# Kernel tuning notes

Hardware: AMD Instinct MI355X
Metric: run time of the kernel (lower is better)

## Reference

```python
import jax, jax.numpy as jnp
import numpy as np

V, E, H = 32000, 256, 256  # vocab, embed dim, encoder hidden (decoder hidden = 2H)
B, S, T = 64, 32, 32


def gru_cell(x, h, W_ih, W_hh, b_ih, b_hh):
    # PyTorch GRU cell math. x: (B, in), h: (B, Hd)
    gi = x @ W_ih.T + b_ih
    gh = h @ W_hh.T + b_hh
    i_r, i_z, i_n = jnp.split(gi, 3, axis=-1)
    h_r, h_z, h_n = jnp.split(gh, 3, axis=-1)
    r = jax.nn.sigmoid(i_r + h_r)
    z = jax.nn.sigmoid(i_z + h_z)
    n = jnp.tanh(i_n + r * h_n)
    return (1.0 - z) * n + z * h


def setup_inputs() -> dict:
    key = jax.random.key(0)
    ks = jax.random.split(key, 20)
    s = 0.05
    emb_enc = jax.random.normal(ks[0], (V, E), jnp.float32) * s
    emb_enc = emb_enc.at[0].set(0.0)  # padding_idx=0
    emb_dec = jax.random.normal(ks[1], (V, E), jnp.float32) * s
    emb_dec = emb_dec.at[0].set(0.0)
    inp = {
        "src": jax.random.randint(ks[2], (B, S), 0, V),
        "trg": jax.random.randint(ks[3], (B, T), 0, V),
        "emb_enc": emb_enc,
        # encoder bidirectional GRU (single layer)
        "W_ih_f": jax.random.normal(ks[4], (3 * H, E), jnp.float32) * s,
        "W_hh_f": jax.random.normal(ks[5], (3 * H, H), jnp.float32) * s,
        "b_ih_f": jnp.zeros((3 * H,), jnp.float32),
        "b_hh_f": jnp.zeros((3 * H,), jnp.float32),
        "W_ih_b": jax.random.normal(ks[6], (3 * H, E), jnp.float32) * s,
        "W_hh_b": jax.random.normal(ks[7], (3 * H, H), jnp.float32) * s,
        "b_ih_b": jnp.zeros((3 * H,), jnp.float32),
        "b_hh_b": jnp.zeros((3 * H,), jnp.float32),
        "emb_dec": emb_dec,
        # decoder GRU: input E + 2H, hidden 2H
        "W_ih_d": jax.random.normal(ks[8], (3 * 2 * H, E + 2 * H), jnp.float32) * s,
        "W_hh_d": jax.random.normal(ks[9], (3 * 2 * H, 2 * H), jnp.float32) * s,
        "b_ih_d": jnp.zeros((3 * 2 * H,), jnp.float32),
        "b_hh_d": jnp.zeros((3 * 2 * H,), jnp.float32),
        "fc_W": jax.random.normal(ks[10], (V, 2 * H), jnp.float32) * s,
        "fc_b": jnp.zeros((V,), jnp.float32),
    }
    return inp


def _forward(src, trg, emb_enc, W_ih_f, W_hh_f, b_ih_f, b_hh_f,
             W_ih_b, W_hh_b, b_ih_b, b_hh_b, emb_dec,
             W_ih_d, W_hh_d, b_ih_d, b_hh_d, fc_W, fc_b):
    b, s = src.shape
    t = trg.shape[1]
    x = emb_enc[src]                      # (B,S,E)
    xs = jnp.swapaxes(x, 0, 1)            # (S,B,E)
    h0 = jnp.zeros((b, H), x.dtype)

    def fstep(h, xt):
        h = gru_cell(xt, h, W_ih_f, W_hh_f, b_ih_f, b_hh_f)
        return h, None

    def bstep(h, xt):
        h = gru_cell(xt, h, W_ih_b, W_hh_b, b_ih_b, b_hh_b)
        return h, None

    hf, _ = jax.lax.scan(fstep, h0, xs)
    hb, _ = jax.lax.scan(bstep, h0, xs[::-1])
    context = jnp.concatenate([hf, hb], axis=-1)   # (B,2H) = final bidir hidden

    # teacher_forcing_ratio = 1.0 -> decoder input at step t is trg[:, t-1]
    dec_in = jnp.swapaxes(trg[:, :-1], 0, 1)       # (T-1, B)

    def dstep(h, tok):
        xt = jnp.concatenate([emb_dec[tok], context], axis=-1)  # (B, E+2H)
        h = gru_cell(xt, h, W_ih_d, W_hh_d, b_ih_d, b_hh_d)
        logits = h @ fc_W.T + fc_b                              # (B, V)
        return h, logits

    _, logits = jax.lax.scan(dstep, context, dec_in)  # (T-1, B, V)
    logits = jnp.swapaxes(logits, 0, 1)                # (B, T-1, V)
    outputs = jnp.concatenate(
        [jnp.zeros((b, 1, fc_W.shape[0]), logits.dtype), logits], axis=1)
    return outputs


def reference(src, trg, emb_enc, W_ih_f, W_hh_f, b_ih_f, b_hh_f,
              W_ih_b, W_hh_b, b_ih_b, b_hh_b, emb_dec,
              W_ih_d, W_hh_d, b_ih_d, b_hh_d, fc_W, fc_b):
    return _forward(src, trg, emb_enc, W_ih_f, W_hh_f, b_ih_f, b_hh_f,
                    W_ih_b, W_hh_b, b_ih_b, b_hh_b, emb_dec,
                    W_ih_d, W_hh_d, b_ih_d, b_hh_d, fc_W, fc_b)
```

## Files before the change

kernel.cpp:

```cpp
#include <hip/hip_runtime.h>
#include <cmath>

typedef _Float16 f16;
typedef _Float16 f16x4 __attribute__((ext_vector_type(4)));
typedef _Float16 f16x8 __attribute__((ext_vector_type(8)));
typedef float f32x4 __attribute__((ext_vector_type(4)));
typedef unsigned u32x4 __attribute__((ext_vector_type(4)));
typedef unsigned long long u64;

static constexpr u64 SENT = 0xFFFFFFFFFFFFFFFFULL;

union V4 { u32x4 u; f16x8 h; };

static constexpr size_t OFF_WIHF = 0;
static constexpr size_t OFF_WHHF = OFF_WIHF + 768UL*256*2;
static constexpr size_t OFF_WIHB = OFF_WHHF + 768UL*256*2;
static constexpr size_t OFF_WHHB = OFF_WIHB + 768UL*256*2;
static constexpr size_t OFF_WIHD = OFF_WHHB + 768UL*256*2;
static constexpr size_t OFF_WHHD = OFF_WIHD + 1536UL*768*2;
static constexpr size_t OFF_FCW  = OFF_WHHD + 1536UL*512*2;
static constexpr size_t OFF_XENC = OFF_FCW  + 32000UL*512*2;
static constexpr size_t OFF_XDEC = OFF_XENC + 2048UL*256*2;
static constexpr size_t OFF_GIF  = OFF_XDEC + 1984UL*256*2;
static constexpr size_t OFF_GIB  = OFF_GIF  + 2048UL*768*4;
static constexpr size_t OFF_GITOK= OFF_GIB  + 2048UL*768*4;
static constexpr size_t OFF_CTX32= OFF_GITOK+ 1984UL*1536*4;
static constexpr size_t OFF_CTX16= OFF_CTX32+ 64UL*512*4;
static constexpr size_t OFF_HPP  = OFF_CTX16+ 64UL*512*2;
static constexpr size_t OFF_HALL = OFF_HPP  + 2UL*32*64*256*2;

__device__ __forceinline__ float sigmoidf_(float x) {
  return __builtin_amdgcn_rcpf(1.f + __expf(-x));
}
__device__ __forceinline__ float tanhf_(float x) {
  float xc = fminf(fmaxf(x, -10.f), 10.f);
  float e = __expf(2.f * xc);
  return (e - 1.f) * __builtin_amdgcn_rcpf(e + 1.f);
}

__device__ __forceinline__ void wait_vm0() {
  asm volatile("s_waitcnt vmcnt(0)" ::: "memory");
  __builtin_amdgcn_sched_barrier(0);
}
__device__ __forceinline__ void sth4(f16* p, float a, float b, float c, float d) {
  union { u64 u; f16 h[4]; } t;
  t.h[0] = (f16)a; t.h[1] = (f16)b; t.h[2] = (f16)c; t.h[3] = (f16)d;
  __hip_atomic_store((u64*)p, t.u, __ATOMIC_RELAXED, __HIP_MEMORY_SCOPE_AGENT);
}

__global__ void k_init(const int* __restrict__ srct, const int* __restrict__ trgt,
                       const float* __restrict__ embe, const float* __restrict__ embd,
                       const float* __restrict__ wihf, const float* __restrict__ whhf,
                       const float* __restrict__ wihb, const float* __restrict__ whhb,
                       const float* __restrict__ wihd, const float* __restrict__ whhd,
                       const float* __restrict__ fcw,
                       f16* dWihf, f16* dWhhf, f16* dWihb, f16* dWhhb,
                       f16* dWihd, f16* dWhhd, f16* dFcw,
                       f16* __restrict__ Xenc, f16* __restrict__ Xdec,
                       f16* __restrict__ hpp, f16* __restrict__ Hall,
                       float* __restrict__ out) {
  int b = blockIdx.x, tid = threadIdx.x;
  if (b < 1024) {
    long t = (long)b * 256 + tid;
    const long stride = 1024L * 256;
    for (long i = t; i < 4032L * 64; i += stride) {
      int row = (int)(i >> 6), j4 = (int)(i & 63);
      const float* e; f16* d; int tok;
      if (row < 2048) {
        int s = row >> 6, bb = row & 63;
        tok = srct[bb * 32 + s]; e = embe; d = Xenc + (long)row * 256;
      } else {
        int rd = row - 2048; int tt = rd >> 6, bb = rd & 63;
        tok = trgt[bb * 32 + tt]; e = embd; d = Xdec + (long)rd * 256;
      }
      float4 v = ((const float4*)(e + (long)tok * 256))[j4];
      f16x4 o; o.x = (f16)v.x; o.y = (f16)v.y; o.z = (f16)v.z; o.w = (f16)v.w;
      ((f16x4*)d)[j4] = o;
    }
    for (long i = t; i < 64L * 8000; i += stride) {
      long bb = i / 8000, j = i % 8000;
      ((float4*)(out + bb * 1024000L))[j] = make_float4(0.f, 0.f, 0.f, 0.f);
    }
    u64* H8 = (u64*)Hall;
    if (t < 253952) H8[t] = SENT;
    u64* P8 = (u64*)hpp;
    if (t < 4096) { P8[t] = 0ULL; P8[131072 + t] = 0ULL; }
    if (t < 126976) { P8[4096 + t] = SENT; P8[131072 + 4096 + t] = SENT; }
  } else {
    long cb = b - 1024;
    const long stride = 4672L * 256;
    for (long i = cb * 256 + tid; i < 4784128L; i += stride) {
      const float* s; f16* d; long j = i;
      if (j < 49152L)        { s = wihf; d = dWihf; }
      else if (j < 98304L)   { s = whhf; d = dWhhf; j -= 49152L; }
      else if (j < 147456L)  { s = wihb; d = dWihb; j -= 98304L; }
      else if (j < 196608L)  { s = whhb; d = dWhhb; j -= 147456L; }
      else if (j < 491520L)  { s = wihd; d = dWihd; j -= 196608L; }
      else if (j < 688128L)  { s = whhd; d = dWhhd; j -= 491520L; }
      else                   { s = fcw;  d = dFcw;  j -= 688128L; }
      float4 v = ((const float4*)s)[j];
      f16x4 o; o.x = (f16)v.x; o.y = (f16)v.y; o.z = (f16)v.z; o.w = (f16)v.w;
      ((f16x4*)d)[j] = o;
    }
  }
}

__device__ __forceinline__ void gemm_body(int bx, int by,
                                          const f16* __restrict__ A, int lda,
                                          const f16* __restrict__ B, int ldb,
                                          const float* __restrict__ bias,
                                          float* __restrict__ C, int ldc, int Ksteps) {
  int m0 = bx * 64, n0 = by * 64;
  int lane = threadIdx.x & 63, w = threadIdx.x >> 6;
  int ar = m0 + w * 16 + (lane & 15);
  int koff = (lane >> 4) * 8;
  f32x4 acc[4] = {};
  for (int ks = 0; ks < Ksteps; ks++) {
    f16x8 a = *(const f16x8*)(A + (size_t)ar * lda + ks * 32 + koff);
#pragma unroll
    for (int ni = 0; ni < 4; ni++) {
      const f16* bp = B + (size_t)(n0 + ni * 16 + (lane & 15)) * ldb + ks * 32 + koff;
      f16x8 bfr = *(const f16x8*)bp;
      acc[ni] = __builtin_amdgcn_mfma_f32_16x16x32_f16(a, bfr, acc[ni], 0, 0, 0);
    }
  }
  int dm = m0 + w * 16 + ((lane >> 4) << 2);
  int dn0 = n0 + (lane & 15);
#pragma unroll
  for (int ni = 0; ni < 4; ni++) {
    int n = dn0 + ni * 16;
    float bv = bias ? bias[n] : 0.f;
#pragma unroll
    for (int r = 0; r < 4; r++) C[(size_t)(dm + r) * ldc + n] = acc[ni][r] + bv;
  }
}

__global__ __launch_bounds__(256) void k_gi(const f16* __restrict__ Xenc, const f16* __restrict__ Xdec,
                                            const f16* __restrict__ Wf, const f16* __restrict__ Wb,
                                            const f16* __restrict__ Wd,
                                            const float* __restrict__ bf, const float* __restrict__ bb,
                                            float* __restrict__ giF, float* __restrict__ giB,
                                            float* __restrict__ giTok) {
  int b = blockIdx.x;
  if (b < 384)      gemm_body(b & 31, b >> 5, Xenc, 256, Wf, 256, bf, giF, 768, 8);
  else if (b < 768) { b -= 384; gemm_body(b & 31, b >> 5, Xenc, 256, Wb, 256, bb, giB, 768, 8); }
  else              { b -= 768; gemm_body(b % 31, b / 31, Xdec, 256, Wd, 768, nullptr, giTok, 1536, 8); }
}

__global__ __launch_bounds__(256, 1) void k_enc(
    const float* __restrict__ giF, const float* __restrict__ giB,
    const f16* __restrict__ WhhF, const f16* __restrict__ WhhB,
    const float* __restrict__ bhhF, const float* __restrict__ bhhB,
    f16* __restrict__ hpp, float* __restrict__ ctx32, f16* __restrict__ ctx16) {
  __shared__ f16 W[96 * 256];
  int wg = blockIdx.x;
  int dir = wg >> 3, ns = wg & 7;
  int tid = threadIdx.x, lane = tid & 63, wv = tid >> 6;
  int mTile = wv;
  const float* gi = dir ? giB : giF;
  const f16* Whh = dir ? WhhB : WhhF;
  const float* bhh = dir ? bhhB : bhhF;
  f16* hb = hpp + (size_t)dir * (32 * 64 * 256);
  int lo = lane & 15, hi = lane >> 4;
  int m = mTile * 16 + lo;
  int jb0 = ns * 32 + hi * 4;

#pragma unroll
  for (int c = 0; c < 12; c++) {
    int seg = c * 256 + tid;
    int row = seg >> 5, ck = seg & 31;
    int q = row >> 5, ii = row & 31;
    f16x8 v = *(const f16x8*)(Whh + (size_t)(q * 256 + ns * 32 + ii) * 256 + ck * 8);
    int col = (ck * 8) ^ ((row & 7) << 3);
    *(f16x8*)&W[row * 256 + col] = v;
  }
  __syncthreads();

  float4 bh[3][2];
#pragma unroll
  for (int q = 0; q < 3; q++)
#pragma unroll
    for (int i = 0; i < 2; i++)
      bh[q][i] = *(const float4*)(bhh + q * 256 + jb0 + i * 16);

  float4 ho[2] = {};
  float4 gcur[3][2];
  {
    int s0 = dir ? 31 : 0;
    const float* g0 = gi + (size_t)s0 * (64 * 768);
#pragma unroll
    for (int q = 0; q < 3; q++)
#pragma unroll
      for (int i = 0; i < 2; i++)
        gcur[q][i] = *(const float4*)(g0 + (size_t)m * 768 + q * 256 + jb0 + i * 16);
  }

  for (int s = 0; s < 32; s++) {
    V4 hv[8];
    const char* hb8 = (const char*)hb + ((size_t)s * 16384 + (size_t)m * 256 + hi * 8) * 2;
    for (;;) {
#pragma unroll
      for (int ks = 0; ks < 8; ks++)
        asm volatile("global_load_dwordx4 %0, %1, off offset:%2 sc0 sc1"
                     : "=&v"(hv[ks].u) : "v"(hb8), "i"(ks * 64));
      wait_vm0();
      unsigned bad = 0;
#pragma unroll
      for (int ks = 0; ks < 8; ks++) {
        bad |= ((hv[ks].u.x & hv[ks].u.y) == 0xFFFFFFFFu);
        bad |= ((hv[ks].u.z & hv[ks].u.w) == 0xFFFFFFFFu);
      }
      if (!__any((int)bad)) break;
      __builtin_amdgcn_s_sleep(1);
    }
    f32x4 acc[3][2] = {};
#pragma unroll
    for (int ks = 0; ks < 8; ks++) {
#pragma unroll
      for (int q = 0; q < 3; q++)
#pragma unroll
        for (int i = 0; i < 2; i++) {
          int row = q * 32 + i * 16 + lo;
          int col = (ks * 32 + hi * 8) ^ ((row & 7) << 3);
          f16x8 w = *(const f16x8*)&W[row * 256 + col];
          acc[q][i] = __builtin_amdgcn_mfma_f32_16x16x32_f16(w, hv[ks].h, acc[q][i], 0, 0, 0);
        }
    }
#pragma unroll
    for (int i = 0; i < 2; i++) {
      float hvv[4];
#pragma unroll
      for (int r2 = 0; r2 < 4; r2++) {
        float rg = sigmoidf_(((const float*)&gcur[0][i])[r2] + acc[0][i][r2] + ((const float*)&bh[0][i])[r2]);
        float zg = sigmoidf_(((const float*)&gcur[1][i])[r2] + acc[1][i][r2] + ((const float*)&bh[1][i])[r2]);
        float ng = tanhf_(((const float*)&gcur[2][i])[r2] + rg * (acc[2][i][r2] + ((const float*)&bh[2][i])[r2]));
        float hprev = ((const float*)&ho[i])[r2];
        hvv[r2] = (1.f - zg) * ng + zg * hprev;
        ((float*)&ho[i])[r2] = hvv[r2];
      }
      if (s < 31) sth4(hb + (size_t)(s + 1) * 16384 + m * 256 + jb0 + i * 16,
                       hvv[0], hvv[1], hvv[2], hvv[3]);
    }
    if (s < 31) {
      int sn = s + 1;
      int sgin = dir ? (31 - sn) : sn;
      const float* gs = gi + (size_t)sgin * (64 * 768);
#pragma unroll
      for (int q = 0; q < 3; q++)
#pragma unroll
        for (int i = 0; i < 2; i++)
          gcur[q][i] = *(const float4*)(gs + (size_t)m * 768 + q * 256 + jb0 + i * 16);
    }
  }
#pragma unroll
  for (int i = 0; i < 2; i++) {
    int c = dir * 256 + jb0 + i * 16;
    *(float4*)(ctx32 + m * 512 + c) = ho[i];
    union { u64 u; f16 h[4]; } t;
#pragma unroll
    for (int r2 = 0; r2 < 4; r2++) t.h[r2] = (f16)((const float*)&ho[i])[r2];
    *(u64*)(ctx16 + m * 512 + c) = t.u;
  }
}

__global__ __launch_bounds__(256, 1) void k_dec(
    const float* __restrict__ giTok, const f16* __restrict__ Wihd, const float* __restrict__ bihd,
    const f16* __restrict__ Whh, const float* __restrict__ bhh,
    const float* __restrict__ ctx32, const f16* __restrict__ ctx16,
    f16* __restrict__ Hall) {
  __shared__ f16 W[48 * 512];
  int cg = blockIdx.x;
  int tid = threadIdx.x, lane = tid & 63, wv = tid >> 6;
  int mTile = wv;
  int lo = lane & 15, hi = lane >> 4;
  int koff = hi * 8;
  int m = mTile * 16 + lo;
  int j0 = cg * 16 + hi * 4;

#pragma unroll
  for (int c = 0; c < 12; c++) {
    int seg = c * 256 + tid;
    int row = seg >> 6, ck = seg & 63;
    int q = row >> 4, ii = row & 15;
    f16x8 v = *(const f16x8*)(Whh + (size_t)(q * 512 + cg * 16 + ii) * 512 + ck * 8);
    int col = (ck * 8) ^ ((row & 7) << 3);
    *(f16x8*)&W[row * 512 + col] = v;
  }

  f32x4 acx[3] = {};
#pragma unroll
  for (int ks = 0; ks < 16; ks++) {
    f16x8 a = *(const f16x8*)(ctx16 + (size_t)m * 512 + ks * 32 + koff);
#pragma unroll
    for (int q = 0; q < 3; q++) {
      f16x8 w = *(const f16x8*)(Wihd + (size_t)(q * 512 + cg * 16 + lo) * 768 + 256 + ks * 32 + koff);
      acx[q] = __builtin_amdgcn_mfma_f32_16x16x32_f16(w, a, acx[q], 0, 0, 0);
    }
  }
  float b0[4], b1[4], bo2[4], bhn[4];
#pragma unroll
  for (int r2 = 0; r2 < 4; r2++) {
    b0[r2]  = acx[0][r2] + bihd[j0 + r2]        + bhh[j0 + r2];
    b1[r2]  = acx[1][r2] + bihd[512 + j0 + r2]  + bhh[512 + j0 + r2];
    bo2[r2] = acx[2][r2] + bihd[1024 + j0 + r2];
    bhn[r2] = bhh[1024 + j0 + r2];
  }
  float4 ho = *(const float4*)(ctx32 + m * 512 + j0);
  float4 gcur[3];
#pragma unroll
  for (int q = 0; q < 3; q++)
    gcur[q] = *(const float4*)(giTok + (size_t)m * 1536 + q * 512 + j0);
  __syncthreads();

  for (int t = 0; t < 31; t++) {
    V4 hv[16];
    if (t == 0) {
      const char* cb = (const char*)ctx16 + ((size_t)m * 512 + hi * 8) * 2;
#pragma unroll
      for (int ks = 0; ks < 16; ks++)
        hv[ks].u = *(const u32x4*)(cb + ks * 64);
    } else {
      const char* hb8 = (const char*)Hall + ((size_t)(t - 1) * 32768 + (size_t)m * 512 + hi * 8) * 2;
      for (;;) {
#pragma unroll
        for (int ks = 0; ks < 16; ks++)
          asm volatile("global_load_dwordx4 %0, %1, off offset:%2 sc0 sc1"
                       : "=&v"(hv[ks].u) : "v"(hb8), "i"(ks * 64));
        wait_vm0();
        unsigned bad = 0;
#pragma unroll
        for (int ks = 0; ks < 16; ks++) {
          bad |= ((hv[ks].u.x & hv[ks].u.y) == 0xFFFFFFFFu);
          bad |= ((hv[ks].u.z & hv[ks].u.w) == 0xFFFFFFFFu);
        }
        if (!__any((int)bad)) break;
        __builtin_amdgcn_s_sleep(1);
      }
    }
    f32x4 acc[3] = {};
#pragma unroll
    for (int ks = 0; ks < 16; ks++) {
#pragma unroll
      for (int q = 0; q < 3; q++) {
        int row = q * 16 + lo;
        int col = (ks * 32 + hi * 8) ^ ((row & 7) << 3);
        f16x8 w = *(const f16x8*)&W[row * 512 + col];
        acc[q] = __builtin_amdgcn_mfma_f32_16x16x32_f16(w, hv[ks].h, acc[q], 0, 0, 0);
      }
    }
    float hvv[4];
#pragma unroll
    for (int r2 = 0; r2 < 4; r2++) {
      float rg = sigmoidf_(((const float*)&gcur[0])[r2] + acc[0][r2] + b0[r2]);
      float zg = sigmoidf_(((const float*)&gcur[1])[r2] + acc[1][r2] + b1[r2]);
      float ng = tanhf_(((const float*)&gcur[2])[r2] + bo2[r2] + rg * (acc[2][r2] + bhn[r2]));
      float hprev = ((const float*)&ho)[r2];
      hvv[r2] = (1.f - zg) * ng + zg * hprev;
      ((float*)&ho)[r2] = hvv[r2];
    }
    sth4(Hall + (size_t)t * 32768 + (size_t)m * 512 + j0, hvv[0], hvv[1], hvv[2], hvv[3]);
    {
      int tn = (t + 1 < 31) ? t + 1 : 30;
      const float* gs = giTok + (size_t)tn * (64 * 1536);
#pragma unroll
      for (int q = 0; q < 3; q++)
        gcur[q] = *(const float4*)(gs + (size_t)m * 1536 + q * 512 + j0);
    }
  }
}

__global__ __launch_bounds__(256, 2) void k_fc(const f16* __restrict__ Hall, const f16* __restrict__ Wfc,
                                               const float* __restrict__ fcb, float* __restrict__ out) {
  __shared__ f16 As[128 * 64];
  __shared__ f16 Bs[128 * 64];
  int bid = blockIdx.x;
  int bx = bid >> 4;
  int by = bid & 15;
  int m0 = by * 128, n0 = bx * 128;
  int tid = threadIdx.x, lane = tid & 63, wv = tid >> 6;
  int wm = wv >> 1, wn = wv & 1;
  f32x4 acc[4][4] = {};
  for (int kk = 0; kk < 8; kk++) {
    f16x8 ra[4], rb[4];
#pragma unroll
    for (int c = 0; c < 4; c++) {
      int seg = c * 256 + tid;
      int row = seg >> 3, ko = (seg & 7) * 8;
      ra[c] = *(const f16x8*)(Hall + (size_t)(m0 + row) * 512 + kk * 64 + ko);
      rb[c] = *(const f16x8*)(Wfc + (size_t)(n0 + row) * 512 + kk * 64 + ko);
    }
    __syncthreads();
#pragma unroll
    for (int c = 0; c < 4; c++) {
      int seg = c * 256 + tid;
      int row = seg >> 3;
      int col = ((seg & 7) * 8) ^ ((row & 7) << 3);
      *(f16x8*)&As[row * 64 + col] = ra[c];
      *(f16x8*)&Bs[row * 64 + col] = rb[c];
    }
    __syncthreads();
#pragma unroll
    for (int ks = 0; ks < 2; ks++) {
      f16x8 af[4], bf[4];
#pragma unroll
      for (int mi = 0; mi < 4; mi++) {
        int row = wm * 64 + mi * 16 + (lane & 15);
        int col = (ks * 32 + (lane >> 4) * 8) ^ ((row & 7) << 3);
        af[mi] = *(const f16x8*)&As[row * 64 + col];
      }
#pragma unroll
      for (int ni = 0; ni < 4; ni++) {
        int row = wn * 64 + ni * 16 + (lane & 15);
        int col = (ks * 32 + (lane >> 4) * 8) ^ ((row & 7) << 3);
        bf[ni] = *(const f16x8*)&Bs[row * 64 + col];
      }
#pragma unroll
      for (int mi = 0; mi < 4; mi++) {
#pragma unroll
        for (int ni = 0; ni < 4; ni++)
          acc[mi][ni] = __builtin_amdgcn_mfma_f32_16x16x32_f16(af[mi], bf[ni], acc[mi][ni], 0, 0, 0);
      }
    }
  }
  int dn0 = n0 + wn * 64 + (lane & 15);
  float bv[4];
#pragma unroll
  for (int ni = 0; ni < 4; ni++) bv[ni] = fcb[dn0 + ni * 16];
#pragma unroll
  for (int mi = 0; mi < 4; mi++) {
    int mbase = m0 + wm * 64 + mi * 16 + ((lane >> 4) << 2);
#pragma unroll
    for (int rr = 0; rr < 4; rr++) {
      int mm = mbase + rr;
      if (mm < 1984) {
        int t = mm >> 6, bb = mm & 63;
        float* orow = out + (size_t)bb * 1024000 + (size_t)(t + 1) * 32000;
#pragma unroll
        for (int ni = 0; ni < 4; ni++)
          __builtin_nontemporal_store(acc[mi][ni][rr] + bv[ni], orow + dn0 + ni * 16);
      }
    }
  }
}

extern "C" void kernel_launch(void* const* d_in, const int* in_sizes, int n_in,
                              void* d_out, int out_size, void* d_ws, size_t ws_size,
                              hipStream_t stream) {
  const int*   srct = (const int*)d_in[0];
  const int*   trgt = (const int*)d_in[1];
  const float* embe = (const float*)d_in[2];
  const float* wihf = (const float*)d_in[3];
  const float* whhf = (const float*)d_in[4];
  const float* bihf = (const float*)d_in[5];
  const float* bhhf = (const float*)d_in[6];
  const float* wihb = (const float*)d_in[7];
  const float* whhb = (const float*)d_in[8];
  const float* bihb = (const float*)d_in[9];
  const float* bhhb = (const float*)d_in[10];
  const float* embd = (const float*)d_in[11];
  const float* wihd = (const float*)d_in[12];
  const float* whhd = (const float*)d_in[13];
  const float* bihd = (const float*)d_in[14];
  const float* bhhd = (const float*)d_in[15];
  const float* fcw  = (const float*)d_in[16];
  const float* fcb  = (const float*)d_in[17];
  float* out = (float*)d_out;
  char* ws = (char*)d_ws;

  f16* W_ihf = (f16*)(ws + OFF_WIHF);
  f16* W_hhf = (f16*)(ws + OFF_WHHF);
  f16* W_ihb = (f16*)(ws + OFF_WIHB);
  f16* W_hhb = (f16*)(ws + OFF_WHHB);
  f16* W_ihd = (f16*)(ws + OFF_WIHD);
  f16* W_hhd = (f16*)(ws + OFF_WHHD);
  f16* Wfc   = (f16*)(ws + OFF_FCW);
  f16* Xenc  = (f16*)(ws + OFF_XENC);
  f16* Xdec  = (f16*)(ws + OFF_XDEC);
  float* giF   = (float*)(ws + OFF_GIF);
  float* giB   = (float*)(ws + OFF_GIB);
  float* giTok = (float*)(ws + OFF_GITOK);
  float* ctx32 = (float*)(ws + OFF_CTX32);
  f16*   ctx16 = (f16*)(ws + OFF_CTX16);
  f16*   hpp   = (f16*)(ws + OFF_HPP);
  f16*   Hall  = (f16*)(ws + OFF_HALL);

  k_init<<<5696, 256, 0, stream>>>(srct, trgt, embe, embd,
                                   wihf, whhf, wihb, whhb, wihd, whhd, fcw,
                                   W_ihf, W_hhf, W_ihb, W_hhb, W_ihd, W_hhd, Wfc,
                                   Xenc, Xdec, hpp, Hall, out);
  k_gi<<<1512, 256, 0, stream>>>(Xenc, Xdec, W_ihf, W_ihb, W_ihd, bihf, bihb,
                                 giF, giB, giTok);
  k_enc<<<16, 256, 0, stream>>>(giF, giB, W_hhf, W_hhb, bhhf, bhhb, hpp, ctx32, ctx16);
  k_dec<<<32, 256, 0, stream>>>(giTok, W_ihd, bihd, W_hhd, bhhd, ctx32, ctx16, Hall);
  k_fc<<<4000, 256, 0, stream>>>(Hall, Wfc, fcb, out);
}
```

Measured before the change: 425.8 us.

## Fuse decoder and FC into one persistent kernel with flag-based overlap

Merges the sequential decoder recurrence and the vocab projection GEMM into a single launch. 32 blocks run the decoder while 224 persistent blocks run FC tiles as soon as the hidden-state rows they need are marked ready through per-block progress flags. The decoder now polls compact flags instead of re-reading sentinel-tagged hidden vectors, and it raises its wave priority. The aim is to hide the FC GEMM behind the latency-bound decoder steps, at the cost of spin-polling traffic and fewer blocks for the GEMM. The encoder also gains a cheap pre-poll before its full sentinel check.

```diff
diff --git a/kernel.cpp b/kernel.cpp
--- a/kernel.cpp
+++ b/kernel.cpp
@@ -28,6 +28,7 @@
 static constexpr size_t OFF_CTX16= OFF_CTX32+ 64UL*512*4;
 static constexpr size_t OFF_HPP  = OFF_CTX16+ 64UL*512*2;
 static constexpr size_t OFF_HALL = OFF_HPP  + 2UL*32*64*256*2;
+static constexpr size_t OFF_FLG  = OFF_HALL + 2048UL*512*2;
 
 __device__ __forceinline__ float sigmoidf_(float x) {
   return __builtin_amdgcn_rcpf(1.f + __expf(-x));
@@ -46,6 +47,22 @@
   union { u64 u; f16 h[4]; } t;
   t.h[0] = (f16)a; t.h[1] = (f16)b; t.h[2] = (f16)c; t.h[3] = (f16)d;
   __hip_atomic_store((u64*)p, t.u, __ATOMIC_RELAXED, __HIP_MEMORY_SCOPE_AGENT);
+}
+__device__ __forceinline__ int ldflag(const int* p) {
+  return __hip_atomic_load(p, __ATOMIC_RELAXED, __HIP_MEMORY_SCOPE_AGENT);
+}
+__device__ __forceinline__ void stflag(int* p, int v) {
+  __hip_atomic_store(p, v, __ATOMIC_RELAXED, __HIP_MEMORY_SCOPE_AGENT);
+}
+__device__ __forceinline__ void pollflags(const int* base, int np, int tgt) {
+  int lane = threadIdx.x & 63;
+  const int* fp = base + lane * 16;
+  for (;;) {
+    int v = (lane < np) ? ldflag(fp) : 0x7fffffff;
+    if (__all(v >= tgt)) break;
+    __builtin_amdgcn_s_sleep(1);
+  }
+  __builtin_amdgcn_sched_barrier(0);
 }
 
 __global__ void k_init(const int* __restrict__ srct, const int* __restrict__ trgt,
@@ -58,7 +75,7 @@
                        f16* dWihd, f16* dWhhd, f16* dFcw,
                        f16* __restrict__ Xenc, f16* __restrict__ Xdec,
                        f16* __restrict__ hpp, f16* __restrict__ Hall,
-                       float* __restrict__ out) {
+                       int* __restrict__ flg, float* __restrict__ out) {
   int b = blockIdx.x, tid = threadIdx.x;
   if (b < 1024) {
     long t = (long)b * 256 + tid;
@@ -86,6 +103,7 @@
     u64* P8 = (u64*)hpp;
     if (t < 4096) { P8[t] = 0ULL; P8[131072 + t] = 0ULL; }
     if (t < 126976) { P8[4096 + t] = SENT; P8[131072 + 4096 + t] = SENT; }
+    if (t < 8192) flg[t] = 0;
   } else {
     long cb = b - 1024;
     const long stride = 4672L * 256;
@@ -195,7 +213,21 @@
         gcur[q][i] = *(const float4*)(g0 + (size_t)m * 768 + q * 256 + jb0 + i * 16);
   }
 
+  const int pj = lane >> 3;
+  const int prow = mTile * 16 + (lane & 7);
+
   for (int s = 0; s < 32; s++) {
+    {
+      const u64* gp = (const u64*)(hb + (size_t)s * 16384) + (size_t)prow * 64 + pj * 8;
+      for (;;) {
+        u64 v;
+        asm volatile("global_load_dwordx2 %0, %1, off sc0 sc1" : "=v"(v) : "v"(gp));
+        asm volatile("s_waitcnt vmcnt(0)" ::: "memory");
+        if (__all((int)(v != SENT))) break;
+        __builtin_amdgcn_s_sleep(1);
+      }
+      __builtin_amdgcn_sched_barrier(0);
+    }
     V4 hv[8];
     const char* hb8 = (const char*)hb + ((size_t)s * 16384 + (size_t)m * 256 + hi * 8) * 2;
     for (;;) {
@@ -263,12 +295,13 @@
   }
 }
 
-__global__ __launch_bounds__(256, 1) void k_dec(
+__device__ __forceinline__ void dec_body(
+    f16* smem,
     const float* __restrict__ giTok, const f16* __restrict__ Wihd, const float* __restrict__ bihd,
     const f16* __restrict__ Whh, const float* __restrict__ bhh,
     const float* __restrict__ ctx32, const f16* __restrict__ ctx16,
-    f16* __restrict__ Hall) {
-  __shared__ f16 W[48 * 512];
+    f16* __restrict__ Hall, int* __restrict__ flg) {
+  f16* W = smem;
   int cg = blockIdx.x;
   int tid = threadIdx.x, lane = tid & 63, wv = tid >> 6;
   int mTile = wv;
@@ -276,6 +309,7 @@
   int koff = hi * 8;
   int m = mTile * 16 + lo;
   int j0 = cg * 16 + hi * 4;
+  __builtin_amdgcn_s_setprio(1);
 
 #pragma unroll
   for (int c = 0; c < 12; c++) {
@@ -312,6 +346,8 @@
     gcur[q] = *(const float4*)(giTok + (size_t)m * 1536 + q * 512 + j0);
   __syncthreads();
 
+  int* gflags = flg + mTile * 512;
+
   for (int t = 0; t < 31; t++) {
     V4 hv[16];
     if (t == 0) {
@@ -320,22 +356,13 @@
       for (int ks = 0; ks < 16; ks++)
         hv[ks].u = *(const u32x4*)(cb + ks * 64);
     } else {
+      pollflags(gflags, 32, t);
       const char* hb8 = (const char*)Hall + ((size_t)(t - 1) * 32768 + (size_t)m * 512 + hi * 8) * 2;
-      for (;;) {
-#pragma unroll
-        for (int ks = 0; ks < 16; ks++)
-          asm volatile("global_load_dwordx4 %0, %1, off offset:%2 sc0 sc1"
-                       : "=&v"(hv[ks].u) : "v"(hb8), "i"(ks * 64));
-        wait_vm0();
-        unsigned bad = 0;
-#pragma unroll
-        for (int ks = 0; ks < 16; ks++) {
-          bad |= ((hv[ks].u.x & hv[ks].u.y) == 0xFFFFFFFFu);
-          bad |= ((hv[ks].u.z & hv[ks].u.w) == 0xFFFFFFFFu);
-        }
-        if (!__any((int)bad)) break;
-        __builtin_amdgcn_s_sleep(1);
-      }
+#pragma unroll
+      for (int ks = 0; ks < 16; ks++)
+        asm volatile("global_load_dwordx4 %0, %1, off offset:%2 sc0 sc1"
+                     : "=&v"(hv[ks].u) : "v"(hb8), "i"(ks * 64));
+      wait_vm0();
     }
     f32x4 acc[3] = {};
 #pragma unroll
@@ -359,6 +386,8 @@
       ((float*)&ho)[r2] = hvv[r2];
     }
     sth4(Hall + (size_t)t * 32768 + (size_t)m * 512 + j0, hvv[0], hvv[1], hvv[2], hvv[3]);
+    wait_vm0();
+    if (lane == 0) stflag(gflags + cg * 16, t + 1);
     {
       int tn = (t + 1 < 31) ? t + 1 : 30;
       const float* gs = giTok + (size_t)tn * (64 * 1536);
@@ -367,80 +396,133 @@
         gcur[q] = *(const float4*)(gs + (size_t)m * 1536 + q * 512 + j0);
     }
   }
-}
-
-__global__ __launch_bounds__(256, 2) void k_fc(const f16* __restrict__ Hall, const f16* __restrict__ Wfc,
-                                               const float* __restrict__ fcb, float* __restrict__ out) {
-  __shared__ f16 As[128 * 64];
-  __shared__ f16 Bs[128 * 64];
-  int bid = blockIdx.x;
-  int bx = bid >> 4;
-  int by = bid & 15;
-  int m0 = by * 128, n0 = bx * 128;
+  __builtin_amdgcn_s_setprio(0);
+}
+
+__device__ __forceinline__ void fc_body(
+    f16* smem,
+    const f16* __restrict__ Hall, const f16* __restrict__ Wfc,
+    const float* __restrict__ fcb, float* __restrict__ out,
+    const int* __restrict__ flg) {
+  f16* As = smem;
+  f16* Bs = smem + 128 * 64;
+  int b = blockIdx.x - 32;
   int tid = threadIdx.x, lane = tid & 63, wv = tid >> 6;
   int wm = wv >> 1, wn = wv & 1;
-  f32x4 acc[4][4] = {};
-  for (int kk = 0; kk < 8; kk++) {
-    f16x8 ra[4], rb[4];
-#pragma unroll
-    for (int c = 0; c < 4; c++) {
-      int seg = c * 256 + tid;
-      int row = seg >> 3, ko = (seg & 7) * 8;
-      ra[c] = *(const f16x8*)(Hall + (size_t)(m0 + row) * 512 + kk * 64 + ko);
-      rb[c] = *(const f16x8*)(Wfc + (size_t)(n0 + row) * 512 + kk * 64 + ko);
+  int lastNeed = 0;
+  const int* fp0 = flg + ((lane >> 5) * 512) + ((lane & 31) * 16);
+  const int* fp1 = flg + (((64 + lane) >> 5) * 512) + ((lane & 31) * 16);
+
+  for (int T = b; T < 4000; T += 224) {
+    int by = T / 250, bx = T % 250;
+    int m0 = by * 128, n0 = bx * 128;
+    int need = (by < 15) ? (2 * by + 2) : 31;
+    if (need > lastNeed) {
+      for (;;) {
+        int v0 = ldflag(fp0), v1 = ldflag(fp1);
+        if (__all((v0 >= need) && (v1 >= need))) break;
+        __builtin_amdgcn_s_sleep(16);
+      }
+      __builtin_amdgcn_sched_barrier(0);
+      lastNeed = need;
+    }
+    f32x4 acc[4][4] = {};
+    for (int kk = 0; kk < 8; kk++) {
+      V4 ra[4]; f16x8 rb[4];
+      bool valid[4];
+#pragma unroll
+      for (int c = 0; c < 4; c++) {
+        int seg = c * 256 + tid;
+        int row = seg >> 3, ko = (seg & 7) * 8;
+        valid[c] = (m0 + row) < 1984;
+        rb[c] = *(const f16x8*)(Wfc + (size_t)(n0 + row) * 512 + kk * 64 + ko);
+      }
+      for (;;) {
+#pragma unroll
+        for (int c = 0; c < 4; c++) {
+          int seg = c * 256 + tid;
+          int row = seg >> 3, ko = (seg & 7) * 8;
+          const char* ap = (const char*)(Hall + (size_t)(m0 + row) * 512 + kk * 64 + ko);
+          asm volatile("global_load_dwordx4 %0, %1, off sc0 sc1" : "=&v"(ra[c].u) : "v"(ap));
+        }
+        wait_vm0();
+        unsigned bad = 0;
+#pragma unroll
+        for (int c = 0; c < 4; c++) {
+          unsigned s1 = ((ra[c].u.x & ra[c].u.y) == 0xFFFFFFFFu);
+          unsigned s2 = ((ra[c].u.z & ra[c].u.w) == 0xFFFFFFFFu);
+          bad |= valid[c] ? (s1 | s2) : 0u;
+        }
+        if (!__any((int)bad)) break;
+        __builtin_amdgcn_s_sleep(1);
+      }
+      __syncthreads();
+#pragma unroll
+      for (int c = 0; c < 4; c++) {
+        int seg = c * 256 + tid;
+        int row = seg >> 3;
+        int col = ((seg & 7) * 8) ^ ((row & 7) << 3);
+        *(f16x8*)&As[row * 64 + col] = ra[c].h;
+        *(f16x8*)&Bs[row * 64 + col] = rb[c];
+      }
+      __syncthreads();
+#pragma unroll
+      for (int ks = 0; ks < 2; ks++) {
+        f16x8 af[4], bf[4];
+#pragma unroll
+        for (int mi = 0; mi < 4; mi++) {
+          int row = wm * 64 + mi * 16 + (lane & 15);
+          int col = (ks * 32 + (lane >> 4) * 8) ^ ((row & 7) << 3);
+          af[mi] = *(const f16x8*)&As[row * 64 + col];
+        }
+#pragma unroll
+        for (int ni = 0; ni < 4; ni++) {
+          int row = wn * 64 + ni * 16 + (lane & 15);
+          int col = (ks * 32 + (lane >> 4) * 8) ^ ((row & 7) << 3);
+          bf[ni] = *(const f16x8*)&Bs[row * 64 + col];
+        }
+#pragma unroll
+        for (int mi = 0; mi < 4; mi++) {
+#pragma unroll
+          for (int ni = 0; ni < 4; ni++)
+            acc[mi][ni] = __builtin_amdgcn_mfma_f32_16x16x32_f16(af[mi], bf[ni], acc[mi][ni], 0, 0, 0);
+        }
+      }
+    }
+    int dn0 = n0 + wn * 64 + (lane & 15);
+    float bv[4];
+#pragma unroll
+    for (int ni = 0; ni < 4; ni++) bv[ni] = fcb[dn0 + ni * 16];
+#pragma unroll
+    for (int mi = 0; mi < 4; mi++) {
+      int mbase = m0 + wm * 64 + mi * 16 + ((lane >> 4) << 2);
+#pragma unroll
+      for (int rr = 0; rr < 4; rr++) {
+        int mm = mbase + rr;
+        if (mm < 1984) {
+          int t = mm >> 6, bb = mm & 63;
+          float* orow = out + (size_t)bb * 1024000 + (size_t)(t + 1) * 32000;
+#pragma unroll
+          for (int ni = 0; ni < 4; ni++)
+            __builtin_nontemporal_store(acc[mi][ni][rr] + bv[ni], orow + dn0 + ni * 16);
+        }
+      }
     }
     __syncthreads();
-#pragma unroll
-    for (int c = 0; c < 4; c++) {
-      int seg = c * 256 + tid;
-      int row = seg >> 3;
-      int col = ((seg & 7) * 8) ^ ((row & 7) << 3);
-      *(f16x8*)&As[row * 64 + col] = ra[c];
-      *(f16x8*)&Bs[row * 64 + col] = rb[c];
-    }
-    __syncthreads();
-#pragma unroll
-    for (int ks = 0; ks < 2; ks++) {
-      f16x8 af[4], bf[4];
-#pragma unroll
-      for (int mi = 0; mi < 4; mi++) {
-        int row = wm * 64 + mi * 16 + (lane & 15);
-        int col = (ks * 32 + (lane >> 4) * 8) ^ ((row & 7) << 3);
-        af[mi] = *(const f16x8*)&As[row * 64 + col];
-      }
-#pragma unroll
-      for (int ni = 0; ni < 4; ni++) {
-        int row = wn * 64 + ni * 16 + (lane & 15);
-        int col = (ks * 32 + (lane >> 4) * 8) ^ ((row & 7) << 3);
-        bf[ni] = *(const f16x8*)&Bs[row * 64 + col];
-      }
-#pragma unroll
-      for (int mi = 0; mi < 4; mi++) {
-#pragma unroll
-        for (int ni = 0; ni < 4; ni++)
-          acc[mi][ni] = __builtin_amdgcn_mfma_f32_16x16x32_f16(af[mi], bf[ni], acc[mi][ni], 0, 0, 0);
-      }
-    }
-  }
-  int dn0 = n0 + wn * 64 + (lane & 15);
-  float bv[4];
-#pragma unroll
-  for (int ni = 0; ni < 4; ni++) bv[ni] = fcb[dn0 + ni * 16];
-#pragma unroll
-  for (int mi = 0; mi < 4; mi++) {
-    int mbase = m0 + wm * 64 + mi * 16 + ((lane >> 4) << 2);
-#pragma unroll
-    for (int rr = 0; rr < 4; rr++) {
-      int mm = mbase + rr;
-      if (mm < 1984) {
-        int t = mm >> 6, bb = mm & 63;
-        float* orow = out + (size_t)bb * 1024000 + (size_t)(t + 1) * 32000;
-#pragma unroll
-        for (int ni = 0; ni < 4; ni++)
-          __builtin_nontemporal_store(acc[mi][ni][rr] + bv[ni], orow + dn0 + ni * 16);
-      }
-    }
-  }
+  }
+}
+
+__global__ __launch_bounds__(256, 1) void k_decfc(
+    const float* __restrict__ giTok, const f16* __restrict__ Wihd, const float* __restrict__ bihd,
+    const f16* __restrict__ Whhd, const float* __restrict__ bhhd,
+    const float* __restrict__ ctx32, const f16* __restrict__ ctx16,
+    f16* __restrict__ Hall, const f16* __restrict__ Wfc, const float* __restrict__ fcb,
+    float* __restrict__ out, int* __restrict__ flg) {
+  __shared__ f16 smem[48 * 512];
+  if (blockIdx.x < 32)
+    dec_body(smem, giTok, Wihd, bihd, Whhd, bhhd, ctx32, ctx16, Hall, flg);
+  else
+    fc_body(smem, Hall, Wfc, fcb, out, flg);
 }
 
 extern "C" void kernel_launch(void* const* d_in, const int* in_sizes, int n_in,
@@ -483,14 +565,15 @@
   f16*   ctx16 = (f16*)(ws + OFF_CTX16);
   f16*   hpp   = (f16*)(ws + OFF_HPP);
   f16*   Hall  = (f16*)(ws + OFF_HALL);
+  int*   flg   = (int*)(ws + OFF_FLG);
 
   k_init<<<5696, 256, 0, stream>>>(srct, trgt, embe, embd,
                                    wihf, whhf, wihb, whhb, wihd, whhd, fcw,
                                    W_ihf, W_hhf, W_ihb, W_hhb, W_ihd, W_hhd, Wfc,
-                                   Xenc, Xdec, hpp, Hall, out);
+                                   Xenc, Xdec, hpp, Hall, flg, out);
   k_gi<<<1512, 256, 0, stream>>>(Xenc, Xdec, W_ihf, W_ihb, W_ihd, bihf, bihb,
                                  giF, giB, giTok);
   k_enc<<<16, 256, 0, stream>>>(giF, giB, W_hhf, W_hhb, bhhf, bhhb, hpp, ctx32, ctx16);
-  k_dec<<<32, 256, 0, stream>>>(giTok, W_ihd, bihd, W_hhd, bhhd, ctx32, ctx16, Hall);
-  k_fc<<<4000, 256, 0, stream>>>(Hall, Wfc, fcb, out);
-}
+  k_decfc<<<256, 256, 0, stream>>>(giTok, W_ihd, bihd, W_hhd, bhhd, ctx32, ctx16,
+                                   Hall, Wfc, fcb, out, flg);
+}
```

After: 447.6 us. +5.1%, slower.
